# Optimization experiments

Hardware: AMD Instinct MI355X
Metric: run time of the kernel (lower is better)

Reference implementation:

```python
import jax, jax.numpy as jnp
import numpy as np

D = 256
K = 3  # depthwise conv kernel size (odd)
A_EPS = 1e-4
POW_MIN = 1e-20
LN_EPS = 1e-5


def setup_inputs() -> dict:
    key = jax.random.key(0)
    ks = jax.random.split(key, 10)
    B, H, W = 8, 96, 96
    x = jax.random.normal(ks[0], (B, H, W, D), dtype=jnp.float32)
    inp = {
        'x': x,
        'ln_g': jnp.ones((D,), jnp.float32),
        'ln_b': jnp.zeros((D,), jnp.float32),
        'w_in': jax.random.normal(ks[1], (D, 2 * D), jnp.float32) * 0.02,
        'b_in': jnp.zeros((2 * D,), jnp.float32),
        'conv_w': jax.random.normal(ks[2], (K, K, 1, D), jnp.float32) * 0.1,
        'conv_b': jnp.zeros((D,), jnp.float32),
        'a_logit': 7.0 + 0.1 * jax.random.normal(ks[3], (D,), jnp.float32),
        'ssm_b': jnp.ones((D,), jnp.float32) + 0.02 * jax.random.normal(ks[4], (D,), jnp.float32),
        'ssm_c': jnp.ones((D,), jnp.float32) + 0.02 * jax.random.normal(ks[5], (D,), jnp.float32),
        'ssm_d': jnp.ones((D,), jnp.float32) + 0.02 * jax.random.normal(ks[6], (D,), jnp.float32),
        'w_out': jax.random.normal(ks[7], (D, D), jnp.float32) * 0.02,
        'b_out': jnp.zeros((D,), jnp.float32),
    }
    return inp


def _ssm_scan(x, a_logit, b, c, d):
    # x: (N, L, D). s_t = a*s_{t-1} + b*x_t ; y_t = c*s_t + d*x_t
    # via log-domain cumsum reformulation (as in the torch source).
    L = x.shape[1]
    a = jnp.clip(jax.nn.sigmoid(a_logit), A_EPS, 1.0 - A_EPS)  # (D,)
    t = jnp.arange(L, dtype=jnp.float32)
    a_pow = jnp.maximum(jnp.exp(t[:, None] * jnp.log(a)[None, :]), POW_MIN)  # (L,D)
    u = x * b  # (N,L,D)
    r = jnp.cumsum(u / a_pow[None], axis=1)
    return r * a_pow[None] * c + x * d


def reference(x, ln_g, ln_b, w_in, b_in, conv_w, conv_b,
              a_logit, ssm_b, ssm_c, ssm_d, w_out, b_out):
    B, H, W, Dm = x.shape
    x0 = x
    # LayerNorm over channel dim
    mu = jnp.mean(x, axis=-1, keepdims=True)
    var = jnp.mean(jnp.square(x - mu), axis=-1, keepdims=True)
    h = (x - mu) * jax.lax.rsqrt(var + LN_EPS) * ln_g + ln_b
    # in_proj -> split into value and gate
    xg = h @ w_in + b_in  # (B,H,W,2D)
    x_in, gate = jnp.split(xg, 2, axis=-1)
    gate = jax.nn.sigmoid(gate)
    # depthwise conv (SAME padding) + SiLU, NHWC layout
    u = jax.lax.conv_general_dilated(
        x_in, conv_w, window_strides=(1, 1), padding='SAME',
        dimension_numbers=('NHWC', 'HWIO', 'NHWC'), feature_group_count=Dm)
    u = jax.nn.silu(u + conv_b)
    # 2D bidirectional scan mixing
    L = H * W
    seq_row = u.reshape(B, L, Dm)
    seq_col = u.transpose(0, 2, 1, 3).reshape(B, L, Dm)

    def bid(s):
        yf = _ssm_scan(s, a_logit, ssm_b, ssm_c, ssm_d)
        yb = jnp.flip(_ssm_scan(jnp.flip(s, axis=1), a_logit, ssm_b, ssm_c, ssm_d), axis=1)
        return 0.5 * (yf + yb)

    y_row = bid(seq_row).reshape(B, H, W, Dm)
    y_col = bid(seq_col).reshape(B, W, H, Dm).transpose(0, 2, 1, 3)
    y = 0.5 * (y_row + y_col)
    # gate, out_proj, residual
    y = y * gate
    y = y @ w_out + b_out
    return x0 + y
```

## Files before the change

### kernel.cpp

```cpp
#include <hip/hip_runtime.h>
#include <math.h>

#define DD   256
#define HHH  96
#define WWW  96
#define NB   8
#define LL   9216
#define NPIX (NB*LL)
#define TCH  32
#define NCH  (LL/TCH)

typedef __bf16 bf16_8 __attribute__((ext_vector_type(8)));
typedef float  f32_4  __attribute__((ext_vector_type(4)));

static __device__ __forceinline__ float sigmoidf_(float x) {
    return 1.0f / (1.0f + expf(-x));
}

typedef const __attribute__((address_space(1))) void gas_void;
typedef __attribute__((address_space(3))) void las_void;
static __device__ __forceinline__ void glld16(const void* g, void* l) {
    __builtin_amdgcn_global_load_lds((gas_void*)g, (las_void*)l, 16, 0, 0);
}

template<int DIR>
static __device__ __forceinline__ int spidx(int t) {
    if (DIR == 0) return t;
    int w = t / HHH;
    int h = t - w * HHH;
    return h * WWW + w;
}

__global__ __launch_bounds__(256) void wcvt_kernel(const float* __restrict__ w_in,
                                                   const float* __restrict__ w_out,
                                                   __bf16* __restrict__ w_inT,
                                                   __bf16* __restrict__ w_outT) {
    int i = blockIdx.x * 256 + threadIdx.x;
    int n = i >> 8, k = i & 255;
    w_inT[i] = (__bf16)w_in[k * 512 + n];
    if (i < 256 * 256) w_outT[i] = (__bf16)w_out[k * 256 + n];
}

__global__ __launch_bounds__(256) void ln_kernel(const float* __restrict__ x,
                                                 const float* __restrict__ g,
                                                 const float* __restrict__ b,
                                                 __bf16* __restrict__ h) {
    int wv = threadIdx.x >> 6, lane = threadIdx.x & 63;
    int pix = blockIdx.x * 4 + wv;
    const float4 v = *(const float4*)&x[(size_t)pix * DD + lane * 4];
    float s  = v.x + v.y + v.z + v.w;
    float s2 = v.x * v.x + v.y * v.y + v.z * v.z + v.w * v.w;
    #pragma unroll
    for (int o = 32; o > 0; o >>= 1) {
        s  += __shfl_xor(s, o, 64);
        s2 += __shfl_xor(s2, o, 64);
    }
    float mu  = s * (1.0f / 256.0f);
    float var = s2 * (1.0f / 256.0f) - mu * mu;
    float r = rsqrtf(var + 1e-5f);
    float4 gg = *(const float4*)&g[lane * 4];
    float4 bb = *(const float4*)&b[lane * 4];
    union { ushort4 u; __bf16 e[4]; } o4;
    o4.e[0] = (__bf16)((v.x - mu) * r * gg.x + bb.x);
    o4.e[1] = (__bf16)((v.y - mu) * r * gg.y + bb.y);
    o4.e[2] = (__bf16)((v.z - mu) * r * gg.z + bb.z);
    o4.e[3] = (__bf16)((v.w - mu) * r * gg.w + bb.w);
    *(ushort4*)&h[(size_t)pix * DD + lane * 4] = o4.u;
}

template<int MODE>
__global__ __launch_bounds__(256) void gemm_bf16(const __bf16* __restrict__ A,
                                                 const __bf16* __restrict__ BT,
                                                 const float* __restrict__ bias,
                                                 __bf16* __restrict__ out_xin,
                                                 __bf16* __restrict__ out_gate,
                                                 float* __restrict__ out_f32,
                                                 const float* __restrict__ x0) {
    const int K = 256;
    const int BK = 32;
    __shared__ __align__(16) char SM[49152];
    auto As = (__bf16 (*)[128 * BK])SM;
    auto Bs = (__bf16 (*)[128 * BK])(SM + 24576);
    int tid = threadIdx.x;
    int lane = tid & 63, wv = tid >> 6;
    int rowBase = blockIdx.x * 128;
    int colBase = blockIdx.y * 128;

    int srow = tid >> 2, sseg = tid & 3;
    const __bf16* aS0 = A  + (size_t)(rowBase + srow) * K + sseg * 8;
    const __bf16* aS1 = A  + (size_t)(rowBase + srow + 64) * K + sseg * 8;
    const __bf16* bS0 = BT + (size_t)(colBase + srow) * K + sseg * 8;
    const __bf16* bS1 = BT + (size_t)(colBase + srow + 64) * K + sseg * 8;
    int wvoff = wv * 1024;

    int m0 = (wv >> 1) * 64, n0 = (wv & 1) * 64;
    int fr = lane & 15, fq = lane >> 4;

    float bvv[4];
    if (MODE == 0) {
        #pragma unroll
        for (int ni = 0; ni < 4; ni++) bvv[ni] = bias[colBase + n0 + ni * 16 + fr];
        asm volatile("" : "+v"(bvv[0]), "+v"(bvv[1]), "+v"(bvv[2]), "+v"(bvv[3]));
    }

#define STAGE(bufi, koff)                                                  \
    do {                                                                   \
        glld16(aS0 + (koff), (char*)&As[bufi][0] + wvoff);                 \
        glld16(aS1 + (koff), (char*)&As[bufi][0] + 4096 + wvoff);          \
        glld16(bS0 + (koff), (char*)&Bs[bufi][0] + wvoff);                 \
        glld16(bS1 + (koff), (char*)&Bs[bufi][0] + 4096 + wvoff);          \
    } while (0)

    STAGE(0, 0);
    STAGE(1, BK);

    f32_4 acc[4][4];
    #pragma unroll
    for (int i = 0; i < 4; i++)
        #pragma unroll
        for (int j = 0; j < 4; j++) acc[i][j] = (f32_4){0.f, 0.f, 0.f, 0.f};

    #pragma unroll
    for (int t = 0; t < 8; ++t) {
        if (t < 7) { asm volatile("s_waitcnt vmcnt(4)" ::: "memory"); }
        else       { asm volatile("s_waitcnt vmcnt(0)" ::: "memory"); }
        __builtin_amdgcn_sched_barrier(0);
        __builtin_amdgcn_s_barrier();
        __builtin_amdgcn_sched_barrier(0);
        if (t + 2 < 8) STAGE((t + 2) % 3, (t + 2) * BK);
        const int cb = t % 3;
        bf16_8 af[4], bb[4];
        #pragma unroll
        for (int mi = 0; mi < 4; mi++)
            af[mi] = *(const bf16_8*)&As[cb][(m0 + mi * 16 + fr) * BK + fq * 8];
        #pragma unroll
        for (int ni = 0; ni < 4; ni++)
            bb[ni] = *(const bf16_8*)&Bs[cb][(n0 + ni * 16 + fr) * BK + fq * 8];
        #pragma unroll
        for (int mi = 0; mi < 4; mi++)
            #pragma unroll
            for (int ni = 0; ni < 4; ni++)
                acc[mi][ni] = __builtin_amdgcn_mfma_f32_16x16x32_bf16(
                    af[mi], bb[ni], acc[mi][ni], 0, 0, 0);
    }
#undef STAGE
    __syncthreads();

    if (MODE == 0) {
        bool gateBlk = (colBase >= 256);
        __bf16* outp = gateBlk ? out_gate : out_xin;
        int colOff = colBase - (gateBlk ? 256 : 0);
        __bf16* eB = (__bf16*)SM;
        #pragma unroll
        for (int c = 0; c < 2; ++c) {
            if ((m0 >> 6) == c) {
                #pragma unroll
                for (int mi = 0; mi < 4; mi++)
                    #pragma unroll
                    for (int ni = 0; ni < 4; ni++)
                        #pragma unroll
                        for (int r = 0; r < 4; r++) {
                            int lr = (m0 & 63) + mi * 16 + fq * 4 + r;
                            float v = acc[mi][ni][r] + bvv[ni];
                            if (gateBlk) v = sigmoidf_(v);
                            eB[lr * 136 + n0 + ni * 16 + fr] = (__bf16)v;
                        }
            }
            __syncthreads();
            #pragma unroll
            for (int i = 0; i < 4; i++) {
                int idx = i * 256 + tid;
                int row = idx >> 4, u8 = idx & 15;
                bf16_8 vv = *(const bf16_8*)&eB[row * 136 + u8 * 8];
                *(bf16_8*)&outp[(size_t)(rowBase + c * 64 + row) * 256
                                + colOff + u8 * 8] = vv;
            }
            __syncthreads();
        }
    } else {
        float* eF = (float*)SM;
        #pragma unroll
        for (int c = 0; c < 4; ++c) {
            #pragma unroll
            for (int mi = 0; mi < 4; mi++) {
                if (((m0 + mi * 16) >> 5) == c) {
                    int lr0 = (m0 + mi * 16) & 31;
                    #pragma unroll
                    for (int ni = 0; ni < 4; ni++)
                        #pragma unroll
                        for (int r = 0; r < 4; r++)
                            eF[(lr0 + fq * 4 + r) * 132 + n0 + ni * 16 + fr]
                                = acc[mi][ni][r];
                }
            }
            __syncthreads();
            #pragma unroll
            for (int i = 0; i < 4; i++) {
                int idx = i * 256 + tid;
                int row = idx >> 5, f4 = idx & 31;
                float4 vv = *(const float4*)&eF[row * 132 + f4 * 4];
                size_t gofs = (size_t)(rowBase + c * 32 + row) * 256
                              + colBase + f4 * 4;
                const float4 xv = *(const float4*)&x0[gofs];
                const float4 bv = *(const float4*)&bias[colBase + f4 * 4];
                vv.x += xv.x + bv.x; vv.y += xv.y + bv.y;
                vv.z += xv.z + bv.z; vv.w += xv.w + bv.w;
                *(float4*)&out_f32[gofs] = vv;
            }
            __syncthreads();
        }
    }
}

static __device__ __forceinline__ void loadcol(const __bf16* __restrict__ xin,
                                               int b, int h, int w, int d,
                                               float c[3]) {
    if (w < 0 || w >= WWW) { c[0] = c[1] = c[2] = 0.f; return; }
    size_t base = ((size_t)b * LL + (size_t)h * WWW + w) * DD + d;
    c[0] = (h > 0)       ? (float)xin[base - (size_t)WWW * DD] : 0.f;
    c[1] = (float)xin[base];
    c[2] = (h + 1 < HHH) ? (float)xin[base + (size_t)WWW * DD] : 0.f;
}

__global__ __launch_bounds__(256) void conv_tot_kernel(const __bf16* __restrict__ xin,
                                                       const float* __restrict__ cw,
                                                       const float* __restrict__ cb,
                                                       const float* __restrict__ a_logit,
                                                       const float* __restrict__ ssm_b,
                                                       __bf16* __restrict__ u,
                                                       float* __restrict__ tot_f,
                                                       float* __restrict__ tot_b) {
    int cx = blockIdx.x, h = blockIdx.y, b = blockIdx.z;
    int d = threadIdx.x;
    int w0 = cx * TCH;
    float k[9];
    #pragma unroll
    for (int i = 0; i < 9; i++) k[i] = cw[i * DD + d];
    float bias = cb[d];
    float a = sigmoidf_(a_logit[d]);
    a = fminf(fmaxf(a, 1e-4f), 1.0f - 1e-4f);
    float bb = ssm_b[d];

    float cl[3], cc[3], cr[3];
    loadcol(xin, b, h, w0 - 1, d, cl);
    loadcol(xin, b, h, w0,     d, cc);
    loadcol(xin, b, h, w0 + 1, d, cr);

    float v[TCH];
    float sf = 0.f;
    size_t outBase = ((size_t)b * LL + (size_t)h * WWW + w0) * DD + d;
    #pragma unroll
    for (int j = 0; j < TCH; j++) {
        float nx[3];
        loadcol(xin, b, h, w0 + j + 2, d, nx);
        float acc = bias;
        acc += k[0] * cl[0] + k[1] * cc[0] + k[2] * cr[0];
        acc += k[3] * cl[1] + k[4] * cc[1] + k[5] * cr[1];
        acc += k[6] * cl[2] + k[7] * cc[2] + k[8] * cr[2];
        float uv = acc * sigmoidf_(acc);
        v[j] = uv;
        u[outBase + (size_t)j * DD] = (__bf16)uv;
        sf = a * sf + bb * uv;
        cl[0] = cc[0]; cl[1] = cc[1]; cl[2] = cc[2];
        cc[0] = cr[0]; cc[1] = cr[1]; cc[2] = cr[2];
        cr[0] = nx[0]; cr[1] = nx[1]; cr[2] = nx[2];
    }
    int chunk = h * 3 + cx;
    tot_f[((size_t)b * NCH + chunk) * DD + d] = sf;
    float sb = 0.f;
    #pragma unroll
    for (int j = TCH - 1; j >= 0; j--) sb = a * sb + bb * v[j];
    tot_b[((size_t)b * NCH + chunk) * DD + d] = sb;
}

__global__ __launch_bounds__(256) void scan_totals_col(const __bf16* __restrict__ u,
                                                       const float* __restrict__ a_logit,
                                                       const float* __restrict__ ssm_b,
                                                       float* __restrict__ tot_f,
                                                       float* __restrict__ tot_b) {
    int blk = blockIdx.x;
    int b = blk / NCH, c = blk - b * NCH;
    int d = threadIdx.x;
    float a = sigmoidf_(a_logit[d]);
    a = fminf(fmaxf(a, 1e-4f), 1.0f - 1e-4f);
    float bb = ssm_b[d];
    size_t base = (size_t)b * LL * DD;
    int t0 = c * TCH;
    float v[TCH];
    #pragma unroll
    for (int j = 0; j < TCH; j++)
        v[j] = (float)u[base + (size_t)spidx<1>(t0 + j) * DD + d];
    float s = 0.f;
    #pragma unroll
    for (int j = 0; j < TCH; j++) s = a * s + bb * v[j];
    tot_f[(size_t)blk * DD + d] = s;
    s = 0.f;
    #pragma unroll
    for (int j = TCH - 1; j >= 0; j--) s = a * s + bb * v[j];
    tot_b[(size_t)blk * DD + d] = s;
}

__global__ __launch_bounds__(256) void scan_carries(const float* __restrict__ tot_all,
                                                    const float* __restrict__ a_logit,
                                                    float* __restrict__ car_all) {
    int b = blockIdx.x;
    int var = blockIdx.y;
    int d = threadIdx.x;
    float a = sigmoidf_(a_logit[d]);
    a = fminf(fmaxf(a, 1e-4f), 1.0f - 1e-4f);
    float a2 = a * a, a4 = a2 * a2, a8 = a4 * a4, a16 = a8 * a8;
    float q = a16 * a16;
    const float* tot = tot_all + (size_t)var * NB * NCH * DD + (size_t)b * NCH * DD + d;
    float* car = car_all + (size_t)var * NB * NCH * DD + (size_t)b * NCH * DD + d;
    float P = 0.f;
    if ((var & 1) == 0) {
        for (int c0 = 0; c0 < NCH; c0 += 8) {
            float t[8];
            #pragma unroll
            for (int j = 0; j < 8; j++) t[j] = tot[(size_t)(c0 + j) * DD];
            #pragma unroll
            for (int j = 0; j < 8; j++) {
                car[(size_t)(c0 + j) * DD] = P;
                P = q * P + t[j];
            }
        }
    } else {
        for (int c0 = NCH - 8; c0 >= 0; c0 -= 8) {
            float t[8];
            #pragma unroll
            for (int j = 0; j < 8; j++) t[j] = tot[(size_t)(c0 + j) * DD];
            #pragma unroll
            for (int j = 7; j >= 0; j--) {
                car[(size_t)(c0 + j) * DD] = P;
                P = q * P + t[j];
            }
        }
    }
}

template<int DIR>
__global__ __launch_bounds__(256) void scan_apply(const __bf16* __restrict__ u,
                                                  const float* __restrict__ a_logit,
                                                  const float* __restrict__ ssm_b,
                                                  const float* __restrict__ ssm_c,
                                                  const float* __restrict__ ssm_d,
                                                  const float* __restrict__ car_f,
                                                  const float* __restrict__ car_b,
                                                  float* __restrict__ y,
                                                  const __bf16* __restrict__ gate,
                                                  __bf16* __restrict__ g) {
    int blk = blockIdx.x;
    int b = blk / NCH, c = blk - b * NCH;
    int d = threadIdx.x;
    float a = sigmoidf_(a_logit[d]);
    a = fminf(fmaxf(a, 1e-4f), 1.0f - 1e-4f);
    float bb = ssm_b[d], cc = ssm_c[d], dd = ssm_d[d];
    size_t base = (size_t)b * LL * DD;
    int t0 = c * TCH;
    float v[TCH];
    #pragma unroll
    for (int j = 0; j < TCH; j++)
        v[j] = (float)u[base + (size_t)spidx<DIR>(t0 + j) * DD + d];
    float yf[TCH];
    float s = car_f[(size_t)blk * DD + d];
    #pragma unroll
    for (int j = 0; j < TCH; j++) {
        s = a * s + bb * v[j];
        yf[j] = cc * s + dd * v[j];
    }
    s = car_b[(size_t)blk * DD + d];
    #pragma unroll
    for (int j = TCH - 1; j >= 0; j--) {
        s = a * s + bb * v[j];
        float val = 0.25f * (yf[j] + cc * s + dd * v[j]);
        size_t idx = base + (size_t)spidx<DIR>(t0 + j) * DD + d;
        if (DIR == 0) {
            y[idx] = val;
        } else {
            float t = y[idx] + val;
            g[idx] = (__bf16)(t * (float)gate[idx]);
        }
    }
}

extern "C" void kernel_launch(void* const* d_in, const int* in_sizes, int n_in,
                              void* d_out, int out_size, void* d_ws, size_t ws_size,
                              hipStream_t stream) {
    const float* x       = (const float*)d_in[0];
    const float* ln_g    = (const float*)d_in[1];
    const float* ln_b    = (const float*)d_in[2];
    const float* w_in    = (const float*)d_in[3];
    const float* b_in    = (const float*)d_in[4];
    const float* conv_w  = (const float*)d_in[5];
    const float* conv_b  = (const float*)d_in[6];
    const float* a_logit = (const float*)d_in[7];
    const float* ssm_b   = (const float*)d_in[8];
    const float* ssm_c   = (const float*)d_in[9];
    const float* ssm_d   = (const float*)d_in[10];
    const float* w_out   = (const float*)d_in[11];
    const float* b_out   = (const float*)d_in[12];
    float* out = (float*)d_out;

    char* ws = (char*)d_ws;
    const size_t SZH = (size_t)NPIX * DD * sizeof(__bf16);
    const size_t TS  = (size_t)NB * NCH * DD * sizeof(float);

    __bf16* hB     = (__bf16*)(ws);
    __bf16* xinB   = (__bf16*)(ws + SZH);
    __bf16* uB     = (__bf16*)(ws + 2 * SZH);
    __bf16* gateB  = (__bf16*)(ws + 3 * SZH);
    float*  tot    = (float*)(ws + 4 * SZH);
    float*  car    = (float*)(ws + 4 * SZH + 4 * TS);
    __bf16* w_inT  = (__bf16*)(ws + 4 * SZH + 8 * TS);
    __bf16* w_outT = w_inT + 512 * 256;
    float* y = out;

    wcvt_kernel<<<512, 256, 0, stream>>>(w_in, w_out, w_inT, w_outT);
    ln_kernel<<<NPIX / 4, 256, 0, stream>>>(x, ln_g, ln_b, hB);
    gemm_bf16<0><<<dim3(NPIX / 128, 4), 256, 0, stream>>>(hB, w_inT, b_in,
                                                          xinB, gateB, nullptr, nullptr);
    conv_tot_kernel<<<dim3(WWW / TCH, HHH, NB), 256, 0, stream>>>(
        xinB, conv_w, conv_b, a_logit, ssm_b, uB,
        tot + 0 * (size_t)NB * NCH * DD, tot + 1 * (size_t)NB * NCH * DD);
    scan_totals_col<<<NB * NCH, 256, 0, stream>>>(
        uB, a_logit, ssm_b,
        tot + 2 * (size_t)NB * NCH * DD, tot + 3 * (size_t)NB * NCH * DD);
    scan_carries<<<dim3(NB, 4), 256, 0, stream>>>(tot, a_logit, car);
    scan_apply<0><<<NB * NCH, 256, 0, stream>>>(
        uB, a_logit, ssm_b, ssm_c, ssm_d,
        car + 0 * (size_t)NB * NCH * DD, car + 1 * (size_t)NB * NCH * DD,
        y, nullptr, nullptr);
    scan_apply<1><<<NB * NCH, 256, 0, stream>>>(
        uB, a_logit, ssm_b, ssm_c, ssm_d,
        car + 2 * (size_t)NB * NCH * DD, car + 3 * (size_t)NB * NCH * DD,
        y, gateB, hB);
    gemm_bf16<1><<<dim3(NPIX / 128, 2), 256, 0, stream>>>(hB, w_outT, b_out,
                                                          nullptr, nullptr, out, x);
}
```

Measured before the change: 373.6 us.

## Widen GEMM tiles to 128x256 and remap block indices across XCDs

Doubles the N-tile of both bf16 GEMMs from 128 to 256 columns, so each block reuses its A tile across more output columns. This halves the number of blocks and removes redundant loads of A. Block IDs are also remapped to a 1D grid, presumably to group neighbouring tiles per XCD for L2 locality. In exchange it uses 72KB of LDS and 128 accumulator registers per thread, which lowers occupancy.

```diff
diff --git a/kernel.cpp b/kernel.cpp
--- a/kernel.cpp
+++ b/kernel.cpp
@@ -78,29 +78,38 @@
                                                  const float* __restrict__ x0) {
     const int K = 256;
     const int BK = 32;
-    __shared__ __align__(16) char SM[49152];
+    const int NXG = (MODE == 0) ? 2 : 1;
+    const int NWG = (NPIX / 128) * NXG;
+    __shared__ __align__(16) char SM[73728];
     auto As = (__bf16 (*)[128 * BK])SM;
-    auto Bs = (__bf16 (*)[128 * BK])(SM + 24576);
+    auto Bs = (__bf16 (*)[256 * BK])(SM + 24576);
     int tid = threadIdx.x;
     int lane = tid & 63, wv = tid >> 6;
-    int rowBase = blockIdx.x * 128;
-    int colBase = blockIdx.y * 128;
+
+    int bid = blockIdx.x;
+    int lg = (bid & 7) * (NWG >> 3) + (bid >> 3);
+    int rowBase = (lg / NXG) * 128;
+    int colBase = (lg % NXG) * 256;
 
     int srow = tid >> 2, sseg = tid & 3;
     const __bf16* aS0 = A  + (size_t)(rowBase + srow) * K + sseg * 8;
-    const __bf16* aS1 = A  + (size_t)(rowBase + srow + 64) * K + sseg * 8;
+    const __bf16* aS1 = aS0 + (size_t)64 * K;
     const __bf16* bS0 = BT + (size_t)(colBase + srow) * K + sseg * 8;
-    const __bf16* bS1 = BT + (size_t)(colBase + srow + 64) * K + sseg * 8;
+    const __bf16* bS1 = bS0 + (size_t)64 * K;
+    const __bf16* bS2 = bS0 + (size_t)128 * K;
+    const __bf16* bS3 = bS0 + (size_t)192 * K;
     int wvoff = wv * 1024;
 
-    int m0 = (wv >> 1) * 64, n0 = (wv & 1) * 64;
+    int m0 = (wv >> 1) * 64;
+    int n0 = (wv & 1) * 128;
     int fr = lane & 15, fq = lane >> 4;
 
-    float bvv[4];
+    float bvv[8];
     if (MODE == 0) {
         #pragma unroll
-        for (int ni = 0; ni < 4; ni++) bvv[ni] = bias[colBase + n0 + ni * 16 + fr];
-        asm volatile("" : "+v"(bvv[0]), "+v"(bvv[1]), "+v"(bvv[2]), "+v"(bvv[3]));
+        for (int ni = 0; ni < 8; ni++) bvv[ni] = bias[colBase + n0 + ni * 16 + fr];
+        #pragma unroll
+        for (int ni = 0; ni < 8; ni++) asm volatile("" : "+v"(bvv[ni]));
     }
 
 #define STAGE(bufi, koff)                                                  \
@@ -109,37 +118,39 @@
         glld16(aS1 + (koff), (char*)&As[bufi][0] + 4096 + wvoff);          \
         glld16(bS0 + (koff), (char*)&Bs[bufi][0] + wvoff);                 \
         glld16(bS1 + (koff), (char*)&Bs[bufi][0] + 4096 + wvoff);          \
+        glld16(bS2 + (koff), (char*)&Bs[bufi][0] + 8192 + wvoff);          \
+        glld16(bS3 + (koff), (char*)&Bs[bufi][0] + 12288 + wvoff);         \
     } while (0)
 
     STAGE(0, 0);
     STAGE(1, BK);
 
-    f32_4 acc[4][4];
+    f32_4 acc[4][8];
     #pragma unroll
     for (int i = 0; i < 4; i++)
         #pragma unroll
-        for (int j = 0; j < 4; j++) acc[i][j] = (f32_4){0.f, 0.f, 0.f, 0.f};
+        for (int j = 0; j < 8; j++) acc[i][j] = (f32_4){0.f, 0.f, 0.f, 0.f};
 
     #pragma unroll
     for (int t = 0; t < 8; ++t) {
-        if (t < 7) { asm volatile("s_waitcnt vmcnt(4)" ::: "memory"); }
+        if (t < 7) { asm volatile("s_waitcnt vmcnt(6)" ::: "memory"); }
         else       { asm volatile("s_waitcnt vmcnt(0)" ::: "memory"); }
         __builtin_amdgcn_sched_barrier(0);
         __builtin_amdgcn_s_barrier();
         __builtin_amdgcn_sched_barrier(0);
         if (t + 2 < 8) STAGE((t + 2) % 3, (t + 2) * BK);
         const int cb = t % 3;
-        bf16_8 af[4], bb[4];
+        bf16_8 af[4], bb[8];
         #pragma unroll
         for (int mi = 0; mi < 4; mi++)
             af[mi] = *(const bf16_8*)&As[cb][(m0 + mi * 16 + fr) * BK + fq * 8];
         #pragma unroll
-        for (int ni = 0; ni < 4; ni++)
+        for (int ni = 0; ni < 8; ni++)
             bb[ni] = *(const bf16_8*)&Bs[cb][(n0 + ni * 16 + fr) * BK + fq * 8];
         #pragma unroll
         for (int mi = 0; mi < 4; mi++)
             #pragma unroll
-            for (int ni = 0; ni < 4; ni++)
+            for (int ni = 0; ni < 8; ni++)
                 acc[mi][ni] = __builtin_amdgcn_mfma_f32_16x16x32_bf16(
                     af[mi], bb[ni], acc[mi][ni], 0, 0, 0);
     }
@@ -149,7 +160,6 @@
     if (MODE == 0) {
         bool gateBlk = (colBase >= 256);
         __bf16* outp = gateBlk ? out_gate : out_xin;
-        int colOff = colBase - (gateBlk ? 256 : 0);
         __bf16* eB = (__bf16*)SM;
         #pragma unroll
         for (int c = 0; c < 2; ++c) {
@@ -157,23 +167,22 @@
                 #pragma unroll
                 for (int mi = 0; mi < 4; mi++)
                     #pragma unroll
-                    for (int ni = 0; ni < 4; ni++)
+                    for (int ni = 0; ni < 8; ni++)
                         #pragma unroll
                         for (int r = 0; r < 4; r++) {
-                            int lr = (m0 & 63) + mi * 16 + fq * 4 + r;
+                            int lr = mi * 16 + fq * 4 + r;
                             float v = acc[mi][ni][r] + bvv[ni];
                             if (gateBlk) v = sigmoidf_(v);
-                            eB[lr * 136 + n0 + ni * 16 + fr] = (__bf16)v;
+                            eB[lr * 264 + n0 + ni * 16 + fr] = (__bf16)v;
                         }
             }
             __syncthreads();
             #pragma unroll
-            for (int i = 0; i < 4; i++) {
+            for (int i = 0; i < 8; i++) {
                 int idx = i * 256 + tid;
-                int row = idx >> 4, u8 = idx & 15;
-                bf16_8 vv = *(const bf16_8*)&eB[row * 136 + u8 * 8];
-                *(bf16_8*)&outp[(size_t)(rowBase + c * 64 + row) * 256
-                                + colOff + u8 * 8] = vv;
+                int row = idx >> 5, u8 = idx & 31;
+                bf16_8 vv = *(const bf16_8*)&eB[row * 264 + u8 * 8];
+                *(bf16_8*)&outp[(size_t)(rowBase + c * 64 + row) * 256 + u8 * 8] = vv;
             }
             __syncthreads();
         }
@@ -186,23 +195,22 @@
                 if (((m0 + mi * 16) >> 5) == c) {
                     int lr0 = (m0 + mi * 16) & 31;
                     #pragma unroll
-                    for (int ni = 0; ni < 4; ni++)
+                    for (int ni = 0; ni < 8; ni++)
                         #pragma unroll
                         for (int r = 0; r < 4; r++)
-                            eF[(lr0 + fq * 4 + r) * 132 + n0 + ni * 16 + fr]
+                            eF[(lr0 + fq * 4 + r) * 260 + n0 + ni * 16 + fr]
                                 = acc[mi][ni][r];
                 }
             }
             __syncthreads();
             #pragma unroll
-            for (int i = 0; i < 4; i++) {
+            for (int i = 0; i < 8; i++) {
                 int idx = i * 256 + tid;
-                int row = idx >> 5, f4 = idx & 31;
-                float4 vv = *(const float4*)&eF[row * 132 + f4 * 4];
-                size_t gofs = (size_t)(rowBase + c * 32 + row) * 256
-                              + colBase + f4 * 4;
+                int row = idx >> 6, f4 = idx & 63;
+                float4 vv = *(const float4*)&eF[row * 260 + f4 * 4];
+                size_t gofs = (size_t)(rowBase + c * 32 + row) * 256 + f4 * 4;
                 const float4 xv = *(const float4*)&x0[gofs];
-                const float4 bv = *(const float4*)&bias[colBase + f4 * 4];
+                const float4 bv = *(const float4*)&bias[f4 * 4];
                 vv.x += xv.x + bv.x; vv.y += xv.y + bv.y;
                 vv.z += xv.z + bv.z; vv.w += xv.w + bv.w;
                 *(float4*)&out_f32[gofs] = vv;
@@ -417,8 +425,8 @@
 
     wcvt_kernel<<<512, 256, 0, stream>>>(w_in, w_out, w_inT, w_outT);
     ln_kernel<<<NPIX / 4, 256, 0, stream>>>(x, ln_g, ln_b, hB);
-    gemm_bf16<0><<<dim3(NPIX / 128, 4), 256, 0, stream>>>(hB, w_inT, b_in,
-                                                          xinB, gateB, nullptr, nullptr);
+    gemm_bf16<0><<<(NPIX / 128) * 2, 256, 0, stream>>>(hB, w_inT, b_in,
+                                                       xinB, gateB, nullptr, nullptr);
     conv_tot_kernel<<<dim3(WWW / TCH, HHH, NB), 256, 0, stream>>>(
         xinB, conv_w, conv_b, a_logit, ssm_b, uB,
         tot + 0 * (size_t)NB * NCH * DD, tot + 1 * (size_t)NB * NCH * DD);
@@ -434,6 +442,6 @@
         uB, a_logit, ssm_b, ssm_c, ssm_d,
         car + 2 * (size_t)NB * NCH * DD, car + 3 * (size_t)NB * NCH * DD,
         y, gateB, hB);
-    gemm_bf16<1><<<dim3(NPIX / 128, 2), 256, 0, stream>>>(hB, w_outT, b_out,
-                                                          nullptr, nullptr, out, x);
-}
+    gemm_bf16<1><<<(NPIX / 128) * 1, 256, 0, stream>>>(hB, w_outT, b_out,
+                                                       nullptr, nullptr, out, x);
+}
```

Result: slower. 454.2 us (+21.6%).
